# Optimization experiments

Measured on AMD Instinct MI355X. Metric: run time of the kernel, lower is better.

The kernel has to match this reference:

```python
import jax, jax.numpy as jnp
import numpy as np

TIME_GAP_BUCKET_COUNT = 64

def setup_inputs() -> dict:
    key = jax.random.key(0)
    ks = jax.random.split(key, 16)
    B, L, H, V, M, G = 32, 512, 256, 100000, 1024, 8
    time_emb = jax.random.normal(ks[8], (TIME_GAP_BUCKET_COUNT + 1, H), jnp.float32) * 0.02
    group_emb = jax.random.normal(ks[9], (G + 1, H), jnp.float32) * 0.02
    return {
        'history_tokens': jax.random.randint(ks[0], (B, L), 0, V, jnp.int32),
        'history_post_tokens': jax.random.randint(ks[1], (B, L), 0, V, jnp.int32),
        'history_author_tokens': jax.random.randint(ks[2], (B, L), 0, V, jnp.int32),
        'history_action_tokens': jax.random.randint(ks[3], (B, L), 0, V, jnp.int32),
        'history_time_gap': jax.random.randint(ks[4], (B, L), 0, TIME_GAP_BUCKET_COUNT + 1, jnp.int32),
        'history_group_ids': jax.random.randint(ks[5], (B, L), 0, G + 1, jnp.int32),
        'history_mask': jax.random.randint(ks[6], (B, L), 0, 2, jnp.int32).astype(bool),
        'token_emb': jax.random.normal(ks[7], (V, H), jnp.float32) * 0.02,
        'time_emb': time_emb.at[0].set(0.0),   # padding_idx=0
        'group_emb': group_emb.at[0].set(0.0),  # padding_idx=0
        'pos_emb': jax.random.normal(ks[10], (M, H), jnp.float32) * 0.02,
        'sep_token': jax.random.normal(ks[11], (H,), jnp.float32) * 0.02,
        'ln_g': jnp.ones((6 * H,), jnp.float32),
        'ln_b': jnp.zeros((6 * H,), jnp.float32),
        'W1': jax.random.normal(ks[12], (6 * H, 4 * H), jnp.float32) * 0.02,
        'b1': jnp.zeros((4 * H,), jnp.float32),
        'W2': jax.random.normal(ks[13], (4 * H, H), jnp.float32) * 0.02,
        'b2': jnp.zeros((H,), jnp.float32),
    }

def _next_valid_group(gid, mask):
    # For each position i, group id of the nearest valid position j > i (or -1).
    B, L = gid.shape
    def step(carry, xm):
        g, m = xm
        return jnp.where(m, g, carry), carry  # emit pre-update carry
    _, nxt = jax.lax.scan(step, jnp.full((B,), -1, gid.dtype),
                          (jnp.flip(gid, 1).T, jnp.flip(mask, 1).T))  # [L,B]
    return jnp.flip(nxt.T, 1)

def reference(history_tokens, history_post_tokens, history_author_tokens,
              history_action_tokens, history_time_gap, history_group_ids,
              history_mask, token_emb, time_emb, group_emb, pos_emb,
              sep_token, ln_g, ln_b, W1, b1, W2, b2):
    M, H = pos_emb.shape
    B, L = history_mask.shape
    # --- event feature assembly ---
    feats = jnp.concatenate([
        token_emb[history_tokens], token_emb[history_post_tokens],
        token_emb[history_author_tokens], token_emb[history_action_tokens],
        time_emb[jnp.clip(history_time_gap, 0, TIME_GAP_BUCKET_COUNT)],
        group_emb[history_group_ids]], axis=-1)  # [B,L,6H]
    mu = feats.mean(-1, keepdims=True)
    var = feats.var(-1, keepdims=True)
    xn = (feats - mu) * jax.lax.rsqrt(var + 1e-5) * ln_g + ln_b
    ev = jax.nn.silu(xn @ W1 + b1) @ W2 + b2  # [B,L,H]
    # --- vectorized merge_with_sep ---
    gid, mask = history_group_ids, history_mask
    nxt = _next_valid_group(gid, mask)
    sep_valid = mask & (nxt >= 0) & (nxt != gid)
    sep_b = jnp.broadcast_to(sep_token, ev.shape)
    tok_c = jnp.stack([ev, sep_b], axis=2).reshape(B, 2 * L, H)   # event, then sep slot
    msk_c = jnp.stack([mask, sep_valid], axis=2).reshape(B, 2 * L)
    rank = jnp.cumsum(msk_c, axis=1) - 1                          # rank among valid pieces
    count = jnp.sum(msk_c, axis=1)                                # pieces per batch
    tgt = M - count[:, None] + rank                               # right-aligned target
    tgt = jnp.where(msk_c & (tgt >= 0), tgt, M)                   # overflow/invalid -> dump slot
    bidx = jnp.arange(B)[:, None]
    merged = jnp.zeros((B, M + 1, H), ev.dtype).at[bidx, tgt].set(
        jnp.where(msk_c[..., None], tok_c, 0.0))[:, :M]
    merged_mask = jnp.zeros((B, M + 1), bool).at[bidx, tgt].set(msk_c)[:, :M]
    merged = (merged + pos_emb[None]) * merged_mask[..., None].astype(ev.dtype)
    return merged, merged_mask
```

## Files before the change

### kernel.cpp

```cpp
#include <hip/hip_runtime.h>
#include <string.h>

#define Hh   256
#define SIXH 1536
#define Bb_  32
#define Ll_  512
#define BL_  16384
#define Mm_  1024
#define N1_  1024
#define K1_  1536
#define K2_  1024
#define N2_  256

typedef __attribute__((ext_vector_type(8))) short bf16x8;
typedef __attribute__((ext_vector_type(4))) float f32x4;

__device__ inline float bf2f(unsigned short u){ unsigned x=(unsigned)u<<16; float f; memcpy(&f,&x,4); return f; }
__device__ inline unsigned short f2bf(float f){ unsigned x; memcpy(&x,&f,4); x = x + 0x7FFFu + ((x>>16)&1u); return (unsigned short)(x>>16); }

#define GL16(gp, lp) __builtin_amdgcn_global_load_lds( \
    (const __attribute__((address_space(1))) void*)(gp), \
    (__attribute__((address_space(3))) void*)(lp), 16, 0, 0)

__global__ __launch_bounds__(512) void fused_pre_kernel(
  const int* __restrict__ tok, const int* __restrict__ post,
  const int* __restrict__ auth, const int* __restrict__ act,
  const int* __restrict__ tg,  const int* __restrict__ gidp,
  const void* __restrict__ maskp,
  const float* __restrict__ token_emb, const float* __restrict__ time_emb,
  const float* __restrict__ group_emb,
  const float* __restrict__ ln_g, const float* __restrict__ ln_b,
  const float* __restrict__ W1, unsigned short* __restrict__ W1t,
  const float* __restrict__ W2, unsigned short* __restrict__ W2t,
  unsigned short* __restrict__ xn,
  int* __restrict__ src, int* __restrict__ count)
{
  int bid = blockIdx.x;
  int t   = threadIdx.x;

  if (bid < 32){
    int b = bid;
    int i = t;
    int lane = i & 63, w = i >> 6;
    bool gt1=false, isf=false;
    for (int k=t;k<4096;k+=512){
      unsigned v=((const unsigned int*)maskp)[k];
      if(v>1u) gt1=true; if(v==0x3F800000u) isf=true;
    }
    __shared__ unsigned long long d1[8], d2[8];
    unsigned long long bg=__ballot(gt1), bff=__ballot(isf);
    if (lane==0){ d1[w]=bg; d2[w]=bff; }
    __syncthreads();
    unsigned long long og=0, of=0;
    #pragma unroll
    for (int k=0;k<8;k++){ og|=d1[k]; of|=d2[k]; }
    int f = og ? (of?2:1) : 0;

    __shared__ int sg[Ll_];
    __shared__ int fv[8];
    __shared__ int wt[8];
    int mv;
    if (f==0)      mv = ((const int*)maskp)[b*Ll_+i];
    else if (f==1) mv = ((const unsigned char*)maskp)[b*Ll_+i];
    else           mv = (((const float*)maskp)[b*Ll_+i] != 0.0f);
    bool m = (mv != 0);
    int g = gidp[b*Ll_+i];
    sg[i] = g;
    unsigned long long W = __ballot(m);
    if (lane==0) fv[w] = W ? (w*64 + __builtin_ctzll(W)) : -1;
    __syncthreads();
    unsigned long long rem = (lane==63) ? 0ull : (W >> (lane+1));
    int nxtpos = -1;
    if (rem) nxtpos = w*64 + lane + 1 + __builtin_ctzll(rem);
    else {
      #pragma unroll
      for (int k=0;k<8;k++)
        if (nxtpos < 0 && k > w && fv[k] >= 0) nxtpos = fv[k];
    }
    int nxt = (nxtpos >= 0) ? sg[nxtpos] : -1;
    bool sep = m && (nxt >= 0) && (nxt != g);
    int ci = (m?1:0) + (sep?1:0);
    int v = ci;
    #pragma unroll
    for (int off=1; off<64; off<<=1){
      int u = __shfl_up(v, off);
      if (lane >= off) v += u;
    }
    if (lane==63) wt[w] = v;
    __syncthreads();
    int woff = 0;
    #pragma unroll
    for (int k=0;k<8;k++) if (k < w) woff += wt[k];
    int e = woff + v - ci;
    int* sb = src + b*Mm_;
    if (m){
      sb[e] = 2*i;
      if (sep) sb[e+1] = 2*i+1;
    }
    if (i==0){
      int tot=0;
      #pragma unroll
      for (int k=0;k<8;k++) tot += wt[k];
      count[b] = tot;
    }
    return;
  }

  if (bid < 928){
    int half = t >> 8;
    int tt = t & 255;
    int id = (bid-32)*2 + half;
    const float* W; unsigned short* Wt; int K, N, tid2;
    if (id < (K1_/32)*(N1_/32)){ W = W1; Wt = W1t; K = K1_; N = N1_; tid2 = id; }
    else { W = W2; Wt = W2t; K = K2_; N = N2_; tid2 = id - (K1_/32)*(N1_/32); }
    __shared__ float tl[2][32][33];
    int ntx = N >> 5;
    int bx = tid2 % ntx;
    int by = tid2 / ntx;
    int tx = tt & 31, ty = tt >> 5;
    #pragma unroll
    for (int i2=0;i2<32;i2+=8)
      tl[half][ty+i2][tx] = W[(size_t)(by*32+ty+i2)*N + bx*32+tx];
    __syncthreads();
    #pragma unroll
    for (int i2=0;i2<32;i2+=8)
      Wt[(size_t)(bx*32+ty+i2)*K + by*32+tx] = f2bf(tl[half][tx][ty+i2]);
    return;
  }

  int rb  = bid - 928;
  int rib = t >> 7;
  int row = rb*4 + rib;
  int wai = (t >> 6) & 1;
  int l   = t & 63;

  int e0 = wai ? post[row] : tok[row];
  int e1 = wai ? act[row]  : auth[row];
  const float* b2p;
  if (wai == 0){
    int i4 = tg[row]; i4 = (i4 < 0) ? 0 : (i4 > 64 ? 64 : i4);
    b2p = time_emb + (size_t)i4*Hh;
  } else {
    b2p = group_emb + (size_t)gidp[row]*Hh;
  }
  const float* b0p = token_emb + (size_t)e0*Hh;
  const float* b1p = token_emb + (size_t)e1*Hh;

  float4 v0 = *(const float4*)(b0p + l*4);
  float4 v1 = *(const float4*)(b1p + l*4);
  float4 v2 = *(const float4*)(b2p + l*4);

  float s  = v0.x+v0.y+v0.z+v0.w + v1.x+v1.y+v1.z+v1.w + v2.x+v2.y+v2.z+v2.w;
  float s2 = v0.x*v0.x+v0.y*v0.y+v0.z*v0.z+v0.w*v0.w
           + v1.x*v1.x+v1.y*v1.y+v1.z*v1.z+v1.w*v1.w
           + v2.x*v2.x+v2.y*v2.y+v2.z*v2.z+v2.w*v2.w;
  #pragma unroll
  for (int off=32; off; off>>=1){ s += __shfl_xor(s,off); s2 += __shfl_xor(s2,off); }

  __shared__ float rs[4][2], rq[4][2];
  if (l==0){ rs[rib][wai] = s; rq[rib][wai] = s2; }
  __syncthreads();
  s  = rs[rib][0] + rs[rib][1];
  s2 = rq[rib][0] + rq[rib][1];
  float mu   = s * (1.0f/1536.0f);
  float var  = s2 * (1.0f/1536.0f) - mu*mu;
  float rstd = rsqrtf(var + 1e-5f);

  unsigned short* xr = xn + (size_t)row*SIXH;
  #pragma unroll
  for (int p=0;p<3;p++){
    int seg = p*2 + wai;
    int j = seg*Hh + l*4;
    float4 g4 = *(const float4*)(ln_g + j);
    float4 bb = *(const float4*)(ln_b + j);
    float4 v = (p==0) ? v0 : (p==1) ? v1 : v2;
    ushort4 o;
    o.x = f2bf((v.x-mu)*rstd*g4.x + bb.x);
    o.y = f2bf((v.y-mu)*rstd*g4.y + bb.y);
    o.z = f2bf((v.z-mu)*rstd*g4.z + bb.z);
    o.w = f2bf((v.w-mu)*rstd*g4.w + bb.w);
    *(ushort4*)(xr + j) = o;
  }
}

__global__ __launch_bounds__(512, 2) void gemm1_cs_kernel(
  const unsigned short* __restrict__ A, const unsigned short* __restrict__ Bt,
  const float* __restrict__ bias, unsigned short* __restrict__ C,
  int M, int N, int K)
{
  __shared__ unsigned short lds[65536];

  int nbx = N >> 8;
  int bid = blockIdx.x;
  if ((gridDim.x & 7) == 0){
    int chunk = gridDim.x >> 3;
    bid = (bid & 7)*chunk + (bid >> 3);
  }
  int bx = bid % nbx, by = bid / nbx;
  int brow = by*256, bcol = bx*256;

  int tid = threadIdx.x, lane = tid & 63, wid = tid >> 6;
  int wr = wid >> 1, wc = wid & 1;

  int sRow = tid >> 3;
  int sSw  = ((tid & 7) ^ (sRow & 7)) << 3;
  const unsigned short* pA0 = A  + (size_t)(brow +   0 + sRow)*K + sSw;
  const unsigned short* pA1 = A  + (size_t)(brow +  64 + sRow)*K + sSw;
  const unsigned short* pA2 = A  + (size_t)(brow + 128 + sRow)*K + sSw;
  const unsigned short* pA3 = A  + (size_t)(brow + 192 + sRow)*K + sSw;
  const unsigned short* pB0 = Bt + (size_t)(bcol +   0 + sRow)*K + sSw;
  const unsigned short* pB1 = Bt + (size_t)(bcol +  64 + sRow)*K + sSw;
  const unsigned short* pB2 = Bt + (size_t)(bcol + 128 + sRow)*K + sSw;
  const unsigned short* pB3 = Bt + (size_t)(bcol + 192 + sRow)*K + sSw;

  int fr = lane & 15, kb = lane >> 4;
  int g0 = (kb ^ (fr & 3)) | (fr & 4);
  int aB = (wr*64  + fr)*64 + g0*8;
  int bB = (wc*128 + fr)*64 + g0*8;

  f32x4 acc[4][8];
  #pragma unroll
  for (int q=0;q<4;q++)
    #pragma unroll
    for (int n=0;n<8;n++) acc[q][n] = (f32x4){0.f,0.f,0.f,0.f};

  bf16x8 a0[4], a1[4], bP[4], bQ[4];

#define ABASE(S) ((S)*16384)
#define BBASE(S) (32768 + (S)*16384)

#define RD_A(buf, S, kc) do{ \
    const unsigned short* L_ = lds + ABASE(S) + (aB ^ ((kc)?32:0)); \
    buf[0] = *(const bf16x8*)(L_); \
    buf[1] = *(const bf16x8*)(L_ + 1024); \
    buf[2] = *(const bf16x8*)(L_ + 2048); \
    buf[3] = *(const bf16x8*)(L_ + 3072); }while(0)

#define RD_B(buf, S, h, kc) do{ \
    const unsigned short* L_ = lds + BBASE(S) + (h)*4096 + (bB ^ ((kc)?32:0)); \
    buf[0] = *(const bf16x8*)(L_); \
    buf[1] = *(const bf16x8*)(L_ + 1024); \
    buf[2] = *(const bf16x8*)(L_ + 2048); \
    buf[3] = *(const bf16x8*)(L_ + 3072); }while(0)

#define STG(p, DB, OFF) GL16((p) + (OFF), lds + (DB) + wid*512)

#define MMX(AF, BF, NB) do{ \
    _Pragma("unroll") for (int q=0;q<4;q++) \
      _Pragma("unroll") for (int nn=0;nn<4;nn++) \
        acc[q][(NB)+nn] = __builtin_amdgcn_mfma_f32_16x16x32_bf16( \
            AF[q], BF[nn], acc[q][(NB)+nn], 0, 0, 0); }while(0)

#define LGKM0 asm volatile("s_waitcnt lgkmcnt(0)" ::: "memory")
#define BAR  __builtin_amdgcn_s_barrier()
#define VM0  asm volatile("s_waitcnt vmcnt(0)" ::: "memory")
#define VNOP do{}while(0)

#define TILE(S, OB1, SP, V4) do{ \
    if (SP){ \
      STG(pA0, ABASE((S)^1) + 0,     OB1); \
      STG(pA1, ABASE((S)^1) + 4096,  OB1); \
      STG(pA2, ABASE((S)^1) + 8192,  OB1); \
      STG(pA3, ABASE((S)^1) + 12288, OB1); \
      STG(pB0, BBASE((S)^1) + 0,     OB1); \
      STG(pB1, BBASE((S)^1) + 4096,  OB1); \
      STG(pB2, BBASE((S)^1) + 8192,  OB1); \
      STG(pB3, BBASE((S)^1) + 12288, OB1); } \
    RD_A(a0, S, 0); RD_B(bP, S, 0, 0); RD_B(bQ, S, 1, 0); \
    MMX(a0, bP, 0); \
    RD_A(a1, S, 1); RD_B(bP, S, 1, 1); \
    MMX(a0, bQ, 4); \
    RD_B(bQ, S, 0, 1); \
    MMX(a1, bP, 4); \
    MMX(a1, bQ, 0); \
    LGKM0; V4; BAR; \
    asm volatile("" ::: "memory"); \
  }while(0)

  int nk = K >> 6;
  STG(pA0, ABASE(0)+0, 0);     STG(pA1, ABASE(0)+4096, 0);
  STG(pA2, ABASE(0)+8192, 0);  STG(pA3, ABASE(0)+12288, 0);
  STG(pB0, BBASE(0)+0, 0);     STG(pB1, BBASE(0)+4096, 0);
  STG(pB2, BBASE(0)+8192, 0);  STG(pB3, BBASE(0)+12288, 0);
  VM0; BAR;
  asm volatile("" ::: "memory");

  for (int tt = 0; tt < (nk-2)/2; ++tt){
    TILE(0,  64, 1, VM0);
    TILE(1, 128, 1, VM0);
    pA0 += 128; pA1 += 128; pA2 += 128; pA3 += 128;
    pB0 += 128; pB1 += 128; pB2 += 128; pB3 += 128;
  }
  TILE(0, 64, 1, VM0);
  TILE(1, 0, 0, VNOP);

#undef TILE
#undef RD_A
#undef RD_B
#undef STG
#undef MMX

  int colb = bcol + wc*128 + fr;
  float bv[8];
  #pragma unroll
  for (int n=0;n<8;n++) bv[n] = bias[colb + n*16];
  int r0 = brow + wr*64 + (lane>>4)*4;
  #pragma unroll
  for (int q=0;q<4;q++){
    #pragma unroll
    for (int j=0;j<4;j++){
      int r = r0 + q*16 + j;
      #pragma unroll
      for (int n=0;n<8;n++){
        float x = acc[q][n][j] + bv[n];
        x = x / (1.0f + expf(-x));
        C[(size_t)r*N + colb + n*16] = f2bf(x);
      }
    }
  }
}

__global__ __launch_bounds__(256) void gemm2_db_kernel(
  const unsigned short* __restrict__ A, const unsigned short* __restrict__ Bt,
  const float* __restrict__ bias, float* __restrict__ C,
  int M, int N, int K)
{
  __shared__ unsigned short lds2[16384];
  int nbx = N >> 6;
  int bid = blockIdx.x;
  if ((gridDim.x & 7) == 0){
    int chunk = gridDim.x >> 3;
    bid = (bid & 7)*chunk + (bid >> 3);
  }
  int bx = bid % nbx, by = bid / nbx;
  int brow = by*64, bcol = bx*64;
  int tid = threadIdx.x, lane = tid & 63, wid = tid >> 6;
  int wr = wid >> 1, wc = wid & 1;

  int srow = tid >> 3;
  int sg   = ((tid & 7) ^ (srow & 7)) << 3;
  const unsigned short* pA0 = A  + (size_t)(brow + srow)*K + sg;
  const unsigned short* pA1 = pA0 + (size_t)32*K;
  const unsigned short* pB0 = Bt + (size_t)(bcol + srow)*K + sg;
  const unsigned short* pB1 = pB0 + (size_t)32*K;

  int fr = lane & 15, kb = lane >> 4;
  int g0 = (kb ^ (fr & 7)) << 3;
  int aB = (wr*32 + fr)*64 + g0;
  int bB = (wc*32 + fr)*64 + g0;

  f32x4 acc[2][2];
  #pragma unroll
  for (int i=0;i<2;i++)
    #pragma unroll
    for (int j=0;j<2;j++) acc[i][j] = (f32x4){0.f,0.f,0.f,0.f};

#define STG2(S, OFF) do{ \
    GL16(pA0 + (OFF), lds2 + (S)*4096 + wid*512); \
    GL16(pA1 + (OFF), lds2 + (S)*4096 + 2048 + wid*512); \
    GL16(pB0 + (OFF), lds2 + 8192 + (S)*4096 + wid*512); \
    GL16(pB1 + (OFF), lds2 + 8192 + (S)*4096 + 2048 + wid*512); }while(0)

  STG2(0, 0);
  asm volatile("s_waitcnt vmcnt(0)" ::: "memory");
  __builtin_amdgcn_s_barrier();
  asm volatile("" ::: "memory");

  int nt = K >> 6;
  for (int t2 = 0; t2 < nt; ++t2){
    int S = t2 & 1;
    if (t2 < nt-1) STG2(S^1, (t2+1)*64);
    bf16x8 a[2][2], b[2][2];
    #pragma unroll
    for (int m=0;m<2;m++)
      #pragma unroll
      for (int kc=0;kc<2;kc++){
        a[m][kc] = *(const bf16x8*)(lds2 + (S)*4096 + ((aB + m*1024) ^ (kc<<5)));
        b[m][kc] = *(const bf16x8*)(lds2 + 8192 + (S)*4096 + ((bB + m*1024) ^ (kc<<5)));
      }
    #pragma unroll
    for (int kc=0;kc<2;kc++)
      #pragma unroll
      for (int m=0;m<2;m++)
        #pragma unroll
        for (int n=0;n<2;n++)
          acc[m][n] = __builtin_amdgcn_mfma_f32_16x16x32_bf16(a[m][kc], b[n][kc], acc[m][n], 0, 0, 0);
    asm volatile("s_waitcnt lgkmcnt(0)" ::: "memory");
    asm volatile("s_waitcnt vmcnt(0)" ::: "memory");
    __builtin_amdgcn_s_barrier();
    asm volatile("" ::: "memory");
  }
#undef STG2

  int col0 = bcol + wc*32 + fr;
  int row0 = brow + wr*32 + (lane >> 4)*4;
  #pragma unroll
  for (int m=0;m<2;m++){
    #pragma unroll
    for (int j=0;j<4;j++){
      int r = row0 + m*16 + j;
      #pragma unroll
      for (int n=0;n<2;n++){
        int c = col0 + n*16;
        C[(size_t)r*N + c] = acc[m][n][j] + bias[c];
      }
    }
  }
}

__global__ __launch_bounds__(256) void output_kernel(
  const float* __restrict__ ev, const float* __restrict__ pos_emb,
  const float* __restrict__ sep_token,
  const int* __restrict__ src, const int* __restrict__ count,
  float* __restrict__ out)
{
  int tid  = threadIdx.x;
  int tpos = blockIdx.x*4 + (tid>>6);
  int lane = tid & 63;
  int b = tpos >> 10;
  int t = tpos & 1023;
  int cnt = count[b];
  int start = Mm_ - cnt;
  float4 val = make_float4(0.f,0.f,0.f,0.f);
  float maskv = 0.f;
  if (t >= start){
    maskv = 1.f;
    int slot = src[b*Mm_ + (t - start)];
    const float* sv = (slot & 1) ? sep_token
                                 : ev + (size_t)(b*Ll_ + (slot>>1))*Hh;
    float4 x = *(const float4*)(sv + lane*4);
    float4 p = *(const float4*)(pos_emb + (size_t)t*Hh + lane*4);
    val = make_float4(x.x+p.x, x.y+p.y, x.z+p.z, x.w+p.w);
  }
  *(float4*)(out + (size_t)tpos*Hh + lane*4) = val;
  if (lane==0) out[(size_t)Bb_*Mm_*Hh + tpos] = maskv;
}

extern "C" void kernel_launch(void* const* d_in, const int* in_sizes, int n_in,
                              void* d_out, int out_size, void* d_ws, size_t ws_size,
                              hipStream_t stream) {
  const int* tok    = (const int*)d_in[0];
  const int* post   = (const int*)d_in[1];
  const int* auth   = (const int*)d_in[2];
  const int* act    = (const int*)d_in[3];
  const int* tg     = (const int*)d_in[4];
  const int* gid    = (const int*)d_in[5];
  const void* maskp =             d_in[6];
  const float* token_emb = (const float*)d_in[7];
  const float* time_emb  = (const float*)d_in[8];
  const float* group_emb = (const float*)d_in[9];
  const float* pos_emb   = (const float*)d_in[10];
  const float* sep_token = (const float*)d_in[11];
  const float* ln_g = (const float*)d_in[12];
  const float* ln_b = (const float*)d_in[13];
  const float* W1   = (const float*)d_in[14];
  const float* b1   = (const float*)d_in[15];
  const float* W2   = (const float*)d_in[16];
  const float* b2   = (const float*)d_in[17];

  char* ws = (char*)d_ws;
  size_t off = 0;
  int* flag = (int*)ws;                                  off += 256;
  unsigned short* xn  = (unsigned short*)(ws + off);     off += (size_t)BL_*SIXH*2;
  unsigned short* h1  = (unsigned short*)(ws + off);     off += (size_t)BL_*N1_*2;
  float*          ev  = (float*)(ws + off);              off += (size_t)BL_*N2_*4;
  unsigned short* w1t = (unsigned short*)(ws + off);     off += (size_t)K1_*N1_*2;
  unsigned short* w2t = (unsigned short*)(ws + off);     off += (size_t)K2_*N2_*2;
  int*            src = (int*)(ws + off);                off += (size_t)Bb_*Mm_*4;
  int*            cnt = (int*)(ws + off);                off += 256;
  (void)flag;

  const int PRE_BLOCKS = 32 + 896 + BL_/4;
  fused_pre_kernel<<<PRE_BLOCKS,512,0,stream>>>(
      tok,post,auth,act,tg,gid, maskp,
      token_emb,time_emb,group_emb, ln_g,ln_b,
      W1,w1t,W2,w2t, xn, src,cnt);
  gemm1_cs_kernel<<<(BL_/256)*(N1_/256),512,0,stream>>>(
      xn, w1t, b1, h1, BL_, N1_, K1_);
  gemm2_db_kernel<<<(BL_/64)*(N2_/64),256,0,stream>>>(
      h1, w2t, b2, ev, BL_, N2_, K2_);
  output_kernel<<<(Bb_*Mm_)/4,256,0,stream>>>(ev, pos_emb, sep_token, src, cnt, (float*)d_out);
}
```

Baseline: 105.9 us.

## Load GEMM1 B operand directly from global into registers, stage only A in LDS

The first GEMM now reads the weight (B) fragments straight from global/L2 into registers each K-step instead of staging them through LDS, halving the LDS buffer to hold only the double-buffered A tile. The A swizzle is simplified to match. This is meant to cut LDS traffic and footprint (possibly raising occupancy), in exchange for redundant global loads of B across waves and blocks and exposed global-load latency inside the MFMA loop.

```diff
diff --git a/kernel.cpp b/kernel.cpp
--- a/kernel.cpp
+++ b/kernel.cpp
@@ -183,12 +183,12 @@
   }
 }
 
-__global__ __launch_bounds__(512, 2) void gemm1_cs_kernel(
+__global__ __launch_bounds__(512, 2) void gemm1_bl2_kernel(
   const unsigned short* __restrict__ A, const unsigned short* __restrict__ Bt,
   const float* __restrict__ bias, unsigned short* __restrict__ C,
   int M, int N, int K)
 {
-  __shared__ unsigned short lds[65536];
+  __shared__ unsigned short lds[32768];
 
   int nbx = N >> 8;
   int bid = blockIdx.x;
@@ -204,19 +204,20 @@
 
   int sRow = tid >> 3;
   int sSw  = ((tid & 7) ^ (sRow & 7)) << 3;
-  const unsigned short* pA0 = A  + (size_t)(brow +   0 + sRow)*K + sSw;
-  const unsigned short* pA1 = A  + (size_t)(brow +  64 + sRow)*K + sSw;
-  const unsigned short* pA2 = A  + (size_t)(brow + 128 + sRow)*K + sSw;
-  const unsigned short* pA3 = A  + (size_t)(brow + 192 + sRow)*K + sSw;
-  const unsigned short* pB0 = Bt + (size_t)(bcol +   0 + sRow)*K + sSw;
-  const unsigned short* pB1 = Bt + (size_t)(bcol +  64 + sRow)*K + sSw;
-  const unsigned short* pB2 = Bt + (size_t)(bcol + 128 + sRow)*K + sSw;
-  const unsigned short* pB3 = Bt + (size_t)(bcol + 192 + sRow)*K + sSw;
+  const unsigned short* pA0 = A + (size_t)(brow +   0 + sRow)*K + sSw;
+  const unsigned short* pA1 = A + (size_t)(brow +  64 + sRow)*K + sSw;
+  const unsigned short* pA2 = A + (size_t)(brow + 128 + sRow)*K + sSw;
+  const unsigned short* pA3 = A + (size_t)(brow + 192 + sRow)*K + sSw;
 
   int fr = lane & 15, kb = lane >> 4;
-  int g0 = (kb ^ (fr & 3)) | (fr & 4);
-  int aB = (wr*64  + fr)*64 + g0*8;
-  int bB = (wc*128 + fr)*64 + g0*8;
+  int g0 = kb ^ (fr & 7);
+  int aB = (wr*64 + fr)*64 + g0*8;
+
+  int frK = fr*K + kb*8;
+  const unsigned short* pB[8];
+  #pragma unroll
+  for (int nn=0;nn<8;nn++)
+    pB[nn] = Bt + (size_t)(bcol + wc*128 + nn*16)*K + frK;
 
   f32x4 acc[4][8];
   #pragma unroll
@@ -224,81 +225,55 @@
     #pragma unroll
     for (int n=0;n<8;n++) acc[q][n] = (f32x4){0.f,0.f,0.f,0.f};
 
-  bf16x8 a0[4], a1[4], bP[4], bQ[4];
-
-#define ABASE(S) ((S)*16384)
-#define BBASE(S) (32768 + (S)*16384)
-
-#define RD_A(buf, S, kc) do{ \
-    const unsigned short* L_ = lds + ABASE(S) + (aB ^ ((kc)?32:0)); \
-    buf[0] = *(const bf16x8*)(L_); \
-    buf[1] = *(const bf16x8*)(L_ + 1024); \
-    buf[2] = *(const bf16x8*)(L_ + 2048); \
-    buf[3] = *(const bf16x8*)(L_ + 3072); }while(0)
-
-#define RD_B(buf, S, h, kc) do{ \
-    const unsigned short* L_ = lds + BBASE(S) + (h)*4096 + (bB ^ ((kc)?32:0)); \
-    buf[0] = *(const bf16x8*)(L_); \
-    buf[1] = *(const bf16x8*)(L_ + 1024); \
-    buf[2] = *(const bf16x8*)(L_ + 2048); \
-    buf[3] = *(const bf16x8*)(L_ + 3072); }while(0)
-
-#define STG(p, DB, OFF) GL16((p) + (OFF), lds + (DB) + wid*512)
-
-#define MMX(AF, BF, NB) do{ \
-    _Pragma("unroll") for (int q=0;q<4;q++) \
-      _Pragma("unroll") for (int nn=0;nn<4;nn++) \
-        acc[q][(NB)+nn] = __builtin_amdgcn_mfma_f32_16x16x32_bf16( \
-            AF[q], BF[nn], acc[q][(NB)+nn], 0, 0, 0); }while(0)
+#define STG_A(S, AOFF) do{ \
+    GL16(pA0 + (AOFF), lds + (S)*16384 +     0 + wid*512); \
+    GL16(pA1 + (AOFF), lds + (S)*16384 +  4096 + wid*512); \
+    GL16(pA2 + (AOFF), lds + (S)*16384 +  8192 + wid*512); \
+    GL16(pA3 + (AOFF), lds + (S)*16384 + 12288 + wid*512); }while(0)
 
 #define LGKM0 asm volatile("s_waitcnt lgkmcnt(0)" ::: "memory")
 #define BAR  __builtin_amdgcn_s_barrier()
 #define VM0  asm volatile("s_waitcnt vmcnt(0)" ::: "memory")
 #define VNOP do{}while(0)
 
-#define TILE(S, OB1, SP, V4) do{ \
-    if (SP){ \
-      STG(pA0, ABASE((S)^1) + 0,     OB1); \
-      STG(pA1, ABASE((S)^1) + 4096,  OB1); \
-      STG(pA2, ABASE((S)^1) + 8192,  OB1); \
-      STG(pA3, ABASE((S)^1) + 12288, OB1); \
-      STG(pB0, BBASE((S)^1) + 0,     OB1); \
-      STG(pB1, BBASE((S)^1) + 4096,  OB1); \
-      STG(pB2, BBASE((S)^1) + 8192,  OB1); \
-      STG(pB3, BBASE((S)^1) + 12288, OB1); } \
-    RD_A(a0, S, 0); RD_B(bP, S, 0, 0); RD_B(bQ, S, 1, 0); \
-    MMX(a0, bP, 0); \
-    RD_A(a1, S, 1); RD_B(bP, S, 1, 1); \
-    MMX(a0, bQ, 4); \
-    RD_B(bQ, S, 0, 1); \
-    MMX(a1, bP, 4); \
-    MMX(a1, bQ, 0); \
+#define TILE(S, BOFF, AOFF, SP, V4) do{ \
+    bf16x8 bF0[8], bF1[8]; \
+    _Pragma("unroll") for (int nn=0;nn<8;nn++){ \
+      bF0[nn] = *(const bf16x8*)((const char*)pB[nn] + (BOFF)); \
+      bF1[nn] = *(const bf16x8*)((const char*)pB[nn] + (BOFF) + 64); } \
+    if (SP) STG_A((S)^1, AOFF); \
+    bf16x8 a_[4]; \
+    _Pragma("unroll") for (int q=0;q<4;q++) \
+      a_[q] = *(const bf16x8*)(lds + (S)*16384 + aB + q*1024); \
+    _Pragma("unroll") for (int q=0;q<4;q++) \
+      _Pragma("unroll") for (int nn=0;nn<8;nn++) \
+        acc[q][nn] = __builtin_amdgcn_mfma_f32_16x16x32_bf16(a_[q], bF0[nn], acc[q][nn], 0, 0, 0); \
+    _Pragma("unroll") for (int q=0;q<4;q++) \
+      a_[q] = *(const bf16x8*)(lds + (S)*16384 + (aB ^ 32) + q*1024); \
+    _Pragma("unroll") for (int q=0;q<4;q++) \
+      _Pragma("unroll") for (int nn=0;nn<8;nn++) \
+        acc[q][nn] = __builtin_amdgcn_mfma_f32_16x16x32_bf16(a_[q], bF1[nn], acc[q][nn], 0, 0, 0); \
     LGKM0; V4; BAR; \
     asm volatile("" ::: "memory"); \
   }while(0)
 
   int nk = K >> 6;
-  STG(pA0, ABASE(0)+0, 0);     STG(pA1, ABASE(0)+4096, 0);
-  STG(pA2, ABASE(0)+8192, 0);  STG(pA3, ABASE(0)+12288, 0);
-  STG(pB0, BBASE(0)+0, 0);     STG(pB1, BBASE(0)+4096, 0);
-  STG(pB2, BBASE(0)+8192, 0);  STG(pB3, BBASE(0)+12288, 0);
+  STG_A(0, 0);
   VM0; BAR;
   asm volatile("" ::: "memory");
 
   for (int tt = 0; tt < (nk-2)/2; ++tt){
-    TILE(0,  64, 1, VM0);
-    TILE(1, 128, 1, VM0);
+    TILE(0,   0,  64, 1, VM0);
+    TILE(1, 128, 128, 1, VM0);
     pA0 += 128; pA1 += 128; pA2 += 128; pA3 += 128;
-    pB0 += 128; pB1 += 128; pB2 += 128; pB3 += 128;
-  }
-  TILE(0, 64, 1, VM0);
-  TILE(1, 0, 0, VNOP);
+    #pragma unroll
+    for (int nn=0;nn<8;nn++) pB[nn] += 128;
+  }
+  TILE(0,   0, 64, 1, VM0);
+  TILE(1, 128,  0, 0, VNOP);
 
 #undef TILE
-#undef RD_A
-#undef RD_B
-#undef STG
-#undef MMX
+#undef STG_A
 
   int colb = bcol + wc*128 + fr;
   float bv[8];
@@ -475,7 +450,7 @@
       tok,post,auth,act,tg,gid, maskp,
       token_emb,time_emb,group_emb, ln_g,ln_b,
       W1,w1t,W2,w2t, xn, src,cnt);
-  gemm1_cs_kernel<<<(BL_/256)*(N1_/256),512,0,stream>>>(
+  gemm1_bl2_kernel<<<(BL_/256)*(N1_/256),512,0,stream>>>(
       xn, w1t, b1, h1, BL_, N1_, K1_);
   gemm2_db_kernel<<<(BL_/64)*(N2_/64),256,0,stream>>>(
       h1, w2t, b2, ev, BL_, N2_, K2_);
```

New measurement: 168.3 us. 59.0% more time.

## Fuse merge scatter and pos-emb add into GEMM2 epilogue, drop ev buffer

Applied to the files above, without the earlier changes.

The preprocessing kernel now computes, for each event, its destination row in the merged output. The second GEMM epilogue then writes bias plus pos_emb straight into that output row instead of storing an intermediate ev buffer. The output kernel becomes a finisher that only zero-fills left padding, writes sep slots and writes the mask. This removes the 16 MB ev write and read round trip. In exchange the GEMM epilogue does scattered non-contiguous stores and extra pos_emb loads.

```diff
diff --git a/kernel.cpp b/kernel.cpp
--- a/kernel.cpp
+++ b/kernel.cpp
@@ -33,7 +33,7 @@
   const float* __restrict__ W1, unsigned short* __restrict__ W1t,
   const float* __restrict__ W2, unsigned short* __restrict__ W2t,
   unsigned short* __restrict__ xn,
-  int* __restrict__ src, int* __restrict__ count)
+  int* __restrict__ src, int* __restrict__ count, int* __restrict__ evdst)
 {
   int bid = blockIdx.x;
   int t   = threadIdx.x;
@@ -88,21 +88,18 @@
     }
     if (lane==63) wt[w] = v;
     __syncthreads();
-    int woff = 0;
-    #pragma unroll
-    for (int k=0;k<8;k++) if (k < w) woff += wt[k];
+    int woff = 0, tot = 0;
+    #pragma unroll
+    for (int k=0;k<8;k++){ if (k < w) woff += wt[k]; tot += wt[k]; }
     int e = woff + v - ci;
+    int start = Mm_ - tot;
     int* sb = src + b*Mm_;
     if (m){
       sb[e] = 2*i;
       if (sep) sb[e+1] = 2*i+1;
     }
-    if (i==0){
-      int tot=0;
-      #pragma unroll
-      for (int k=0;k<8;k++) tot += wt[k];
-      count[b] = tot;
-    }
+    evdst[b*Ll_+i] = m ? (b*Mm_ + start + e) : -1;
+    if (i==0) count[b] = tot;
     return;
   }
 
@@ -320,9 +317,10 @@
   }
 }
 
-__global__ __launch_bounds__(256) void gemm2_db_kernel(
+__global__ __launch_bounds__(256) void gemm2_scatter_kernel(
   const unsigned short* __restrict__ A, const unsigned short* __restrict__ Bt,
-  const float* __restrict__ bias, float* __restrict__ C,
+  const float* __restrict__ bias, const int* __restrict__ evdst,
+  const float* __restrict__ pos_emb, float* __restrict__ out,
   int M, int N, int K)
 {
   __shared__ unsigned short lds2[16384];
@@ -399,19 +397,23 @@
     #pragma unroll
     for (int j=0;j<4;j++){
       int r = row0 + m*16 + j;
-      #pragma unroll
-      for (int n=0;n<2;n++){
-        int c = col0 + n*16;
-        C[(size_t)r*N + c] = acc[m][n][j] + bias[c];
+      int d = evdst[r];
+      if (d >= 0){
+        const float* pe = pos_emb + (size_t)(d & (Mm_-1))*Hh;
+        float* orow = out + (size_t)d*Hh;
+        #pragma unroll
+        for (int n=0;n<2;n++){
+          int c = col0 + n*16;
+          orow[c] = acc[m][n][j] + bias[c] + pe[c];
+        }
       }
     }
   }
 }
 
-__global__ __launch_bounds__(256) void output_kernel(
-  const float* __restrict__ ev, const float* __restrict__ pos_emb,
-  const float* __restrict__ sep_token,
+__global__ __launch_bounds__(256) void finisher_kernel(
   const int* __restrict__ src, const int* __restrict__ count,
+  const float* __restrict__ sep_token, const float* __restrict__ pos_emb,
   float* __restrict__ out)
 {
   int tid  = threadIdx.x;
@@ -421,18 +423,20 @@
   int t = tpos & 1023;
   int cnt = count[b];
   int start = Mm_ - cnt;
-  float4 val = make_float4(0.f,0.f,0.f,0.f);
-  float maskv = 0.f;
-  if (t >= start){
+  float maskv;
+  if (t < start){
+    maskv = 0.f;
+    *(float4*)(out + (size_t)tpos*Hh + lane*4) = make_float4(0.f,0.f,0.f,0.f);
+  } else {
     maskv = 1.f;
     int slot = src[b*Mm_ + (t - start)];
-    const float* sv = (slot & 1) ? sep_token
-                                 : ev + (size_t)(b*Ll_ + (slot>>1))*Hh;
-    float4 x = *(const float4*)(sv + lane*4);
-    float4 p = *(const float4*)(pos_emb + (size_t)t*Hh + lane*4);
-    val = make_float4(x.x+p.x, x.y+p.y, x.z+p.z, x.w+p.w);
-  }
-  *(float4*)(out + (size_t)tpos*Hh + lane*4) = val;
+    if (slot & 1){
+      float4 x = *(const float4*)(sep_token + lane*4);
+      float4 p = *(const float4*)(pos_emb + (size_t)t*Hh + lane*4);
+      *(float4*)(out + (size_t)tpos*Hh + lane*4) =
+          make_float4(x.x+p.x, x.y+p.y, x.z+p.z, x.w+p.w);
+    }
+  }
   if (lane==0) out[(size_t)Bb_*Mm_*Hh + tpos] = maskv;
 }
 
@@ -463,7 +467,7 @@
   int* flag = (int*)ws;                                  off += 256;
   unsigned short* xn  = (unsigned short*)(ws + off);     off += (size_t)BL_*SIXH*2;
   unsigned short* h1  = (unsigned short*)(ws + off);     off += (size_t)BL_*N1_*2;
-  float*          ev  = (float*)(ws + off);              off += (size_t)BL_*N2_*4;
+  int*            evdst = (int*)(ws + off);              off += (size_t)BL_*4;
   unsigned short* w1t = (unsigned short*)(ws + off);     off += (size_t)K1_*N1_*2;
   unsigned short* w2t = (unsigned short*)(ws + off);     off += (size_t)K2_*N2_*2;
   int*            src = (int*)(ws + off);                off += (size_t)Bb_*Mm_*4;
@@ -474,10 +478,11 @@
   fused_pre_kernel<<<PRE_BLOCKS,512,0,stream>>>(
       tok,post,auth,act,tg,gid, maskp,
       token_emb,time_emb,group_emb, ln_g,ln_b,
-      W1,w1t,W2,w2t, xn, src,cnt);
+      W1,w1t,W2,w2t, xn, src,cnt, evdst);
   gemm1_cs_kernel<<<(BL_/256)*(N1_/256),512,0,stream>>>(
       xn, w1t, b1, h1, BL_, N1_, K1_);
-  gemm2_db_kernel<<<(BL_/64)*(N2_/64),256,0,stream>>>(
-      h1, w2t, b2, ev, BL_, N2_, K2_);
-  output_kernel<<<(Bb_*Mm_)/4,256,0,stream>>>(ev, pos_emb, sep_token, src, cnt, (float*)d_out);
+  gemm2_scatter_kernel<<<(BL_/64)*(N2_/64),256,0,stream>>>(
+      h1, w2t, b2, evdst, pos_emb, (float*)d_out, BL_, N2_, K2_);
+  finisher_kernel<<<(Bb_*Mm_)/4,256,0,stream>>>(src, cnt, sep_token, pos_emb,
+                                                (float*)d_out);
 }
```

New measurement: 107.8 us. About the same (+1.9%).
